# Kernel tuning notes

Measured on AMD Instinct MI355X. Metric: run time of the kernel, lower is better.

The kernel has to match this reference:

```python
import jax, jax.numpy as jnp
import numpy as np

B, N, F, Tf, Tm, Df, Dm = 8, 128, 128, 64, 256, 32, 128
E, H, TE = 64, 128, 64  # node_emb_dim, hidden_dim, time_emb_dim


def setup_inputs() -> dict:
    key = jax.random.key(0)
    ks = jax.random.split(key, 16)
    s = 0.05
    return {
        'noisy_adj': jax.random.normal(ks[0], (B, N, N), jnp.float32),
        'node_feats': jax.random.normal(ks[1], (B, N, F), jnp.float32),
        'feat_fnirs': jax.random.normal(ks[2], (B, N, Tf, Df), jnp.float32),
        'feat_music': jax.random.normal(ks[3], (B, 1, Tm, Dm), jnp.float32),
        'g_pre': jax.random.normal(ks[4], (B, N, N), jnp.float32),
        'node_W': jax.random.normal(ks[5], (F, E), jnp.float32) * s,
        'node_b': jnp.zeros((E,), jnp.float32),
        'fnirs_W': jax.random.normal(ks[6], (Df, H), jnp.float32) * s,
        'fnirs_b': jnp.zeros((H,), jnp.float32),
        'music_W': jax.random.normal(ks[7], (Dm, H), jnp.float32) * s,
        'music_b': jnp.zeros((H,), jnp.float32),
        'mlp_W1': jax.random.normal(ks[8], (2 * E + 2 + H + TE, H), jnp.float32) * s,
        'mlp_b1': jnp.zeros((H,), jnp.float32),
        'mlp_W2': jax.random.normal(ks[9], (H, 1), jnp.float32) * s,
        'mlp_b2': jnp.zeros((1,), jnp.float32),
        't': jax.random.randint(ks[10], (B,), 0, Tf),
    }


def _time_embedding(t_idx):
    # sinusoidal timestep embedding -> [B, TE]
    half = TE // 2
    inv_freq = jnp.exp(-jnp.arange(half, dtype=jnp.float32) * (jnp.log(10000.0) / (half - 1)))
    freqs = t_idx.astype(jnp.float32)[:, None] * inv_freq  # [B, half]
    return jnp.concatenate([jnp.sin(freqs), jnp.cos(freqs)], axis=-1)


def _conditional(feat_fnirs, feat_music, fnirs_W, fnirs_b, music_W, music_b):
    # cross-attention: fNIRS timesteps attend over music timesteps
    q = feat_fnirs @ fnirs_W + fnirs_b          # [B,N,Tf,H]
    kv = feat_music @ music_W + music_b         # [B,1,Tm,H]
    scale = 1.0 / jnp.sqrt(jnp.float32(H))
    scores = jnp.einsum('bnfh,bomh->bnfm', q, kv) * scale  # [B,N,Tf,Tm]
    attn = jax.nn.softmax(scores, axis=-1)
    ctx = jnp.einsum('bnfm,bomh->bnfh', attn, kv)
    fused = q + ctx                              # [B,N,Tf,H]
    attn_weights = attn.mean(axis=1)             # mean across channels -> [B,Tf,Tm]
    ent = -(attn * jnp.log(attn + 1e-8)).sum(-1)
    attention_loss = ent.mean()
    return fused, attn_weights, attention_loss


def reference(noisy_adj, node_feats, feat_fnirs, feat_music, g_pre,
              node_W, node_b, fnirs_W, fnirs_b, music_W, music_b,
              mlp_W1, mlp_b1, mlp_W2, mlp_b2, t):
    h = node_feats @ node_W + node_b             # [B,N,E]

    fused, attn_weights, attention_loss = _conditional(
        feat_fnirs, feat_music, fnirs_W, fnirs_b, music_W, music_b)

    t_idx = jnp.clip(t, 0, fused.shape[2] - 1)
    # gather conditional state at diffusion step t -> [B,N,H]
    idx = jnp.broadcast_to(t_idx[:, None, None, None], (B, N, 1, H))
    cond_t = jnp.take_along_axis(fused, idx, axis=2)[:, :, 0, :]

    time_emb = _time_embedding(t_idx)            # [B,TE]

    # Fused edge MLP layer-1: split W1 along the concat axis instead of
    # materializing the [B,N,N,in_dim] concat tensor (same math).
    W1_hi = mlp_W1[:E]
    W1_hj = mlp_W1[E:2 * E]
    w_adj = mlp_W1[2 * E]          # [H]
    w_gpre = mlp_W1[2 * E + 1]     # [H]
    W1_cond = mlp_W1[2 * E + 2:2 * E + 2 + H]
    W1_time = mlp_W1[2 * E + 2 + H:]

    pre = ((h @ W1_hi)[:, :, None, :]            # h_i varies over row i
           + (h @ W1_hj)[:, None, :, :]          # h_j varies over col j
           + noisy_adj[..., None] * w_adj
           + g_pre[..., None] * w_gpre
           + (cond_t @ W1_cond)[:, None, :, :]   # cond broadcast over row i
           + (time_emb @ W1_time)[:, None, None, :]
           + mlp_b1)                             # [B,N,N,H]
    hid = jax.nn.relu(pre)
    noise_pred = (hid @ mlp_W2)[..., 0] + mlp_b2[0]  # [B,N,N]
    return noise_pred, attn_weights, attention_loss
```

## Files before the change

kernel.cpp:

```cpp
#include <hip/hip_runtime.h>
#include <hip/hip_bf16.h>

#define Bn  8
#define Nn  128
#define Fn  128
#define Tfn 64
#define Tmn 256
#define Dfn 32
#define Dmn 128
#define En  64
#define Hn  128
#define TEn 64

#define OUT_AW_OFF   (Bn*Nn*Nn)
#define OUT_LOSS_OFF (Bn*Nn*Nn + Bn*Tfn*Tmn)

#define WS_KV    0
#define WS_GBF   (WS_KV + Bn*Tmn*Hn)
#define WS_BIAS  (WS_GBF + (Bn*Tmn*Dfn)/2)
#define WS_PI    (WS_BIAS + Bn*Tmn)
#define WS_PJ    (WS_PI + Bn*Nn*Hn)
#define WS_LOSS  (WS_PJ + Bn*Nn*Hn)

#define SCALE 0.08838834764831845f

typedef __attribute__((ext_vector_type(8))) short short8;
typedef __attribute__((ext_vector_type(4))) float f32x4;

__device__ __forceinline__ unsigned short f2bf(float x) {
  __hip_bfloat16 h = __float2bfloat16(x);
  return __builtin_bit_cast(unsigned short, h);
}
__device__ __forceinline__ unsigned int pk2(float a, float b) {
  return (unsigned int)f2bf(a) | ((unsigned int)f2bf(b) << 16);
}
__device__ __forceinline__ float bfl(unsigned int u) {
  union { unsigned int u; float f; } v; v.u = u << 16; return v.f;
}
__device__ __forceinline__ float bfh(unsigned int u) {
  union { unsigned int u; float f; } v; v.u = u & 0xFFFF0000u; return v.f;
}

__global__ __launch_bounds__(128) void k_kv(
    const float* __restrict__ feat_music, const float* __restrict__ music_W,
    const float* __restrict__ music_b, const float* __restrict__ fnirs_W,
    const float* __restrict__ fnirs_b, float* __restrict__ kv,
    unsigned short* __restrict__ G_bf, float* __restrict__ bias,
    float* __restrict__ loss_acc)
{
  int b = blockIdx.x >> 8;
  int m = blockIdx.x & 255;
  int tid = threadIdx.x;
  __shared__ float fm_s[Dmn];
  __shared__ float kv_s[Hn];
  fm_s[tid] = feat_music[((size_t)b*Tmn + m)*Dmn + tid];
  __syncthreads();
  float a = music_b[tid];
  #pragma unroll 8
  for (int d = 0; d < Dmn; d++) a = fmaf(fm_s[d], music_W[d*Hn + tid], a);
  kv[((size_t)b*Tmn + m)*Hn + tid] = a;
  kv_s[tid] = a;
  __syncthreads();
  if (tid < Dfn) {
    float g = 0.f;
    #pragma unroll 8
    for (int h = 0; h < Hn; h++) g = fmaf(fnirs_W[tid*Hn + h], kv_s[h], g);
    G_bf[((size_t)b*Tmn + m)*Dfn + tid] = f2bf(g * SCALE);
  } else if (tid == 64) {
    float g = 0.f;
    #pragma unroll 8
    for (int h = 0; h < Hn; h++) g = fmaf(fnirs_b[h], kv_s[h], g);
    bias[(size_t)b*Tmn + m] = g * SCALE;
  }
  if (blockIdx.x == 0 && tid == 0) loss_acc[0] = 0.f;
}

__global__ __launch_bounds__(256, 2) void k_attn(
    const float* __restrict__ feat_fnirs, const unsigned short* __restrict__ G_bf,
    const float* __restrict__ bias, float* __restrict__ aw_out,
    float* __restrict__ loss_acc)
{
  __shared__ unsigned short feat_l[Nn][40];
  __shared__ unsigned short G_l[Tmn][40];
  __shared__ float bias_l[Tmn];
  __shared__ float aw_l[4][Tmn];
  __shared__ float ent_l[4];

  int tid = threadIdx.x;
  int b = blockIdx.x >> 6, f = blockIdx.x & 63;

  {
    const uint4* gg = (const uint4*)(G_bf + (size_t)b*Tmn*Dfn);
    #pragma unroll
    for (int v0 = 0; v0 < 4; v0++) {
      int v = tid + v0*256;
      uint4 x = gg[v];
      int m = v >> 2, qt = v & 3;
      *((uint4*)&G_l[m][qt*8]) = x;
    }
    bias_l[tid] = bias[b*Tmn + tid];
    int n = tid >> 1, hf = tid & 1;
    const float* src = feat_fnirs + (((size_t)b*Nn + n)*Tfn + f)*Dfn + hf*16;
    float4 x0 = ((const float4*)src)[0];
    float4 x1 = ((const float4*)src)[1];
    float4 x2 = ((const float4*)src)[2];
    float4 x3 = ((const float4*)src)[3];
    uint4 pa, pb;
    pa.x = pk2(x0.x, x0.y); pa.y = pk2(x0.z, x0.w);
    pa.z = pk2(x1.x, x1.y); pa.w = pk2(x1.z, x1.w);
    pb.x = pk2(x2.x, x2.y); pb.y = pk2(x2.z, x2.w);
    pb.z = pk2(x3.x, x3.y); pb.w = pk2(x3.z, x3.w);
    uint4* dst = (uint4*)&feat_l[n][hf*16];
    dst[0] = pa; dst[1] = pb;
  }
  __syncthreads();

  int lane = tid & 63, wv = tid >> 6;
  int col = lane & 15, kq = lane >> 4;
  int n0 = wv * 32;

  short8 a0 = *(const short8*)&feat_l[n0 + col][kq*8];
  short8 a1 = *(const short8*)&feat_l[n0 + 16 + col][kq*8];

  float S0[4] = {0,0,0,0}, S1[4] = {0,0,0,0};
  float T0[4] = {0,0,0,0}, T1[4] = {0,0,0,0};
  float p0[16][4], p1[16][4];

  #pragma unroll
  for (int mt = 0; mt < 16; mt++) {
    short8 bfr = *(const short8*)&G_l[mt*16 + col][kq*8];
    float bv = bias_l[mt*16 + col];
    f32x4 c0 = __builtin_amdgcn_mfma_f32_16x16x32_bf16(a0, bfr, (f32x4){0.f,0.f,0.f,0.f}, 0, 0, 0);
    f32x4 c1 = __builtin_amdgcn_mfma_f32_16x16x32_bf16(a1, bfr, (f32x4){0.f,0.f,0.f,0.f}, 0, 0, 0);
    #pragma unroll
    for (int r = 0; r < 4; r++) {
      float sc = c0[r] + bv;
      float p = __expf(sc);
      S0[r] += p; T0[r] = fmaf(p, sc, T0[r]); p0[mt][r] = p;
      sc = c1[r] + bv;
      p = __expf(sc);
      S1[r] += p; T1[r] = fmaf(p, sc, T1[r]); p1[mt][r] = p;
    }
  }

  #pragma unroll
  for (int r = 0; r < 4; r++) {
    #pragma unroll
    for (int off = 1; off < 16; off <<= 1) {
      S0[r] += __shfl_xor(S0[r], off);
      S1[r] += __shfl_xor(S1[r], off);
      T0[r] += __shfl_xor(T0[r], off);
      T1[r] += __shfl_xor(T1[r], off);
    }
  }
  float i0v[4], i1v[4];
  #pragma unroll
  for (int r = 0; r < 4; r++) { i0v[r] = 1.f / S0[r]; i1v[r] = 1.f / S1[r]; }

  float ent = 0.f;
  if (col == 0) {
    #pragma unroll
    for (int r = 0; r < 4; r++) {
      ent += (__logf(S0[r]) - T0[r] * i0v[r]);
      ent += (__logf(S1[r]) - T1[r] * i1v[r]);
    }
  }
  ent += __shfl_xor(ent, 32); ent += __shfl_xor(ent, 16);
  ent += __shfl_xor(ent, 8);  ent += __shfl_xor(ent, 4);
  ent += __shfl_xor(ent, 2);  ent += __shfl_xor(ent, 1);
  if (lane == 0) ent_l[wv] = ent;

  #pragma unroll
  for (int mt = 0; mt < 16; mt++) {
    float a = 0.f;
    #pragma unroll
    for (int r = 0; r < 4; r++) {
      a = fmaf(p0[mt][r], i0v[r], a);
      a = fmaf(p1[mt][r], i1v[r], a);
    }
    a += __shfl_xor(a, 16);
    a += __shfl_xor(a, 32);
    if (lane < 16) aw_l[wv][mt*16 + lane] = a;
  }
  __syncthreads();

  float s = (aw_l[0][tid] + aw_l[1][tid]) + (aw_l[2][tid] + aw_l[3][tid]);
  aw_out[((size_t)b*Tfn + f)*Tmn + tid] = s * (1.f/(float)Nn);
  if (tid == 0)
    atomicAdd(loss_acc, (ent_l[0] + ent_l[1]) + (ent_l[2] + ent_l[3]));
}

__global__ __launch_bounds__(128) void k_cond(
    const float* __restrict__ feat_fnirs, const float* __restrict__ fnirs_W,
    const float* __restrict__ fnirs_b, const float* __restrict__ kv,
    const unsigned short* __restrict__ G_bf, const float* __restrict__ bias,
    const int* __restrict__ t, const float* __restrict__ node_feats,
    const float* __restrict__ node_W, const float* __restrict__ node_b,
    const float* __restrict__ W1, const float* __restrict__ b1,
    float* __restrict__ Pi, float* __restrict__ Pj)
{
  int b = blockIdx.x >> 7, i = blockIdx.x & 127;
  int tid = threadIdx.x;
  int tcl = min(max(t[b], 0), Tfn - 1);
  __shared__ float feat_s[Dfn], attn_s[Tmn], nf_s[Fn], h_s[En], cond_s[Hn],
                   te_s[TEn], red_s[2];

  nf_s[tid] = node_feats[((size_t)b*Nn + i)*Fn + tid];
  if (tid < Dfn) feat_s[tid] = feat_fnirs[(((size_t)b*Nn + i)*Tfn + tcl)*Dfn + tid];
  if (tid >= 64 && tid < 96) {
    int u = tid - 64;
    float fr = (float)tcl * __expf(-(float)u * (logf(10000.f) / (TEn/2 - 1)));
    te_s[u] = __sinf(fr);
    te_s[u + TEn/2] = __cosf(fr);
  }
  __syncthreads();

  {
    float sc0 = bias[b*Tmn + tid], sc1 = bias[b*Tmn + tid + 128];
    const unsigned short* r0 = G_bf + ((size_t)b*Tmn + tid)*Dfn;
    const unsigned short* r1 = G_bf + ((size_t)b*Tmn + tid + 128)*Dfn;
    #pragma unroll 8
    for (int d = 0; d < Dfn; d += 2) {
      unsigned int w0 = *(const unsigned int*)(r0 + d);
      unsigned int w1 = *(const unsigned int*)(r1 + d);
      sc0 = fmaf(feat_s[d], bfl(w0), sc0); sc0 = fmaf(feat_s[d+1], bfh(w0), sc0);
      sc1 = fmaf(feat_s[d], bfl(w1), sc1); sc1 = fmaf(feat_s[d+1], bfh(w1), sc1);
    }
    float p0 = __expf(sc0), p1 = __expf(sc1);
    float v = p0 + p1;
    v += __shfl_xor(v, 32); v += __shfl_xor(v, 16); v += __shfl_xor(v, 8);
    v += __shfl_xor(v, 4);  v += __shfl_xor(v, 2);  v += __shfl_xor(v, 1);
    if ((tid & 63) == 0) red_s[tid >> 6] = v;
    __syncthreads();
    float invS = 1.f / (red_s[0] + red_s[1]);
    attn_s[tid] = p0 * invS;
    attn_s[tid + 128] = p1 * invS;
  }

  if (tid < En) {
    float a = node_b[tid];
    #pragma unroll 8
    for (int ff = 0; ff < Fn; ff++) a = fmaf(nf_s[ff], node_W[ff*En + tid], a);
    h_s[tid] = a;
  }
  __syncthreads();

  float q = fnirs_b[tid];
  #pragma unroll 8
  for (int d = 0; d < Dfn; d++) q = fmaf(feat_s[d], fnirs_W[d*Hn + tid], q);
  float ctx = 0.f;
  const float* kvb = kv + (size_t)b*Tmn*Hn + tid;
  #pragma unroll 8
  for (int m = 0; m < Tmn; m++) ctx = fmaf(attn_s[m], kvb[(size_t)m*Hn], ctx);
  cond_s[tid] = q + ctx;
  __syncthreads();

  int k = tid;
  float A = 0.f, Bv = 0.f, C = 0.f, Dv = 0.f;
  #pragma unroll 4
  for (int e = 0; e < En; e++) {
    float hv = h_s[e];
    A  = fmaf(hv, W1[e*Hn + k], A);
    Bv = fmaf(hv, W1[(En + e)*Hn + k], Bv);
  }
  #pragma unroll 4
  for (int c = 0; c < Hn; c++) C = fmaf(cond_s[c], W1[(2*En + 2 + c)*Hn + k], C);
  #pragma unroll 4
  for (int u = 0; u < TEn; u++) Dv = fmaf(te_s[u], W1[(2*En + 2 + Hn + u)*Hn + k], Dv);
  Pi[((size_t)b*Nn + i)*Hn + k] = A;
  Pj[((size_t)b*Nn + i)*Hn + k] = Bv + C + Dv + b1[k];
}

__global__ __launch_bounds__(256) void k_edge(
    const float* __restrict__ adj, const float* __restrict__ gpre,
    const float* __restrict__ W1, const float* __restrict__ W2,
    const float* __restrict__ b2p, const float* __restrict__ Pi,
    const float* __restrict__ Pj, float* __restrict__ out,
    const float* __restrict__ loss_acc)
{
  int b  = blockIdx.x >> 6;
  int ib = (blockIdx.x >> 1) & 31;
  int jh = blockIdx.x & 1;
  int i0 = ib * 4;
  int tid = threadIdx.x;

  __shared__ float4 Pj_s4[64*32];
  __shared__ float4 Pi_s4[4*32];
  __shared__ float4 w2_s[32], wa_s[32], wg_s[32];

  {
    const float4* Pjg = (const float4*)(Pj + ((size_t)b*Nn + jh*64)*Hn);
    #pragma unroll
    for (int v0 = 0; v0 < 8; v0++) {
      int idx = tid + v0*256;
      int j = idx >> 5, c = idx & 31;
      Pj_s4[j*32 + (c ^ (j & 7))] = Pjg[j*32 + c];
    }
    if (tid < 128) {
      int r = tid >> 5, c = tid & 31;
      Pi_s4[r*32 + c] = ((const float4*)(Pi + ((size_t)b*Nn + i0 + r)*Hn))[c];
    } else if (tid < 160) {
      int c = tid - 128;
      w2_s[c] = ((const float4*)W2)[c];
      wa_s[c] = ((const float4*)(W1 + (2*En)*Hn))[c];
      wg_s[c] = ((const float4*)(W1 + (2*En + 1)*Hn))[c];
    }
  }
  __syncthreads();

  int r = tid >> 6, lane = tid & 63;
  int i = i0 + r, j = jh*64 + lane;
  float b2v = b2p[0];
  float adjv = adj [((size_t)b*Nn + i)*Nn + j];
  float gpv  = gpre[((size_t)b*Nn + i)*Nn + j];
  float a0 = 0.f, a1 = 0.f, a2 = 0.f, a3 = 0.f;
  #pragma unroll
  for (int c = 0; c < 32; c++) {
    float4 pj = Pj_s4[lane*32 + (c ^ (lane & 7))];
    float4 pi = Pi_s4[r*32 + c];
    float4 wa = wa_s[c], wg = wg_s[c], w2 = w2_s[c];
    float e0 = pi.x + pj.x + adjv*wa.x + gpv*wg.x;
    float e1 = pi.y + pj.y + adjv*wa.y + gpv*wg.y;
    float e2 = pi.z + pj.z + adjv*wa.z + gpv*wg.z;
    float e3 = pi.w + pj.w + adjv*wa.w + gpv*wg.w;
    a0 = fmaf(fmaxf(e0, 0.f), w2.x, a0);
    a1 = fmaf(fmaxf(e1, 0.f), w2.y, a1);
    a2 = fmaf(fmaxf(e2, 0.f), w2.z, a2);
    a3 = fmaf(fmaxf(e3, 0.f), w2.w, a3);
  }
  out[((size_t)b*Nn + i)*Nn + j] = (a0 + a1) + (a2 + a3) + b2v;

  if (blockIdx.x == 0 && tid == 0)
    out[OUT_LOSS_OFF] = loss_acc[0] * (1.f / (float)(Bn*Nn*Tfn));
}

extern "C" void kernel_launch(void* const* d_in, const int* in_sizes, int n_in,
                              void* d_out, int out_size, void* d_ws, size_t ws_size,
                              hipStream_t stream) {
  (void)in_sizes; (void)n_in; (void)out_size; (void)ws_size;
  const float* noisy_adj  = (const float*)d_in[0];
  const float* node_feats = (const float*)d_in[1];
  const float* feat_fnirs = (const float*)d_in[2];
  const float* feat_music = (const float*)d_in[3];
  const float* g_pre      = (const float*)d_in[4];
  const float* node_W     = (const float*)d_in[5];
  const float* node_b     = (const float*)d_in[6];
  const float* fnirs_W    = (const float*)d_in[7];
  const float* fnirs_b    = (const float*)d_in[8];
  const float* music_W    = (const float*)d_in[9];
  const float* music_b    = (const float*)d_in[10];
  const float* mlp_W1     = (const float*)d_in[11];
  const float* mlp_b1     = (const float*)d_in[12];
  const float* mlp_W2     = (const float*)d_in[13];
  const float* mlp_b2     = (const float*)d_in[14];
  const int*   t          = (const int*)d_in[15];

  float* out = (float*)d_out;
  float* ws = (float*)d_ws;
  float*          kv_ws   = ws + WS_KV;
  unsigned short* gbf_ws  = (unsigned short*)(ws + WS_GBF);
  float*          bias_ws = ws + WS_BIAS;
  float*          Pi_ws   = ws + WS_PI;
  float*          Pj_ws   = ws + WS_PJ;
  float*          loss_ws = ws + WS_LOSS;

  k_kv  <<<Bn*Tmn, 128, 0, stream>>>(feat_music, music_W, music_b, fnirs_W,
                                     fnirs_b, kv_ws, gbf_ws, bias_ws, loss_ws);
  k_attn<<<Bn*Tfn, 256, 0, stream>>>(feat_fnirs, gbf_ws, bias_ws,
                                     out + OUT_AW_OFF, loss_ws);
  k_cond<<<Bn*Nn,  128, 0, stream>>>(feat_fnirs, fnirs_W, fnirs_b, kv_ws,
                                     gbf_ws, bias_ws, t, node_feats, node_W,
                                     node_b, mlp_W1, mlp_b1, Pi_ws, Pj_ws);
  k_edge<<<512,    256, 0, stream>>>(noisy_adj, g_pre, mlp_W1, mlp_W2, mlp_b2,
                                     Pi_ws, Pj_ws, out, loss_ws);
}
```

Measured before the change: 158.6 us.

## Rewrite conditional projection kernel with bf16 MFMA over 16-node tiles

Replaces the per-node scalar k_cond with a 16-node tile kernel that uses bf16 MFMA for the scores, the softmax-weighted context, the node embedding and the W1 projections. A new prep kernel transposes and casts the weights to bf16 and precomputes the time-embedding term. k_kv now writes a transposed bf16 kv and parallelises the G/bias reductions across more threads. The aim is to cut the scalar FMA work and the repeated weight reads in k_cond, at the cost of an extra launch and bf16 rounding of cond and h.

```diff
diff --git a/kernel.cpp b/kernel.cpp
--- a/kernel.cpp
+++ b/kernel.cpp
@@ -15,12 +15,18 @@
 #define OUT_AW_OFF   (Bn*Nn*Nn)
 #define OUT_LOSS_OFF (Bn*Nn*Nn + Bn*Tfn*Tmn)
 
-#define WS_KV    0
-#define WS_GBF   (WS_KV + Bn*Tmn*Hn)
-#define WS_BIAS  (WS_GBF + (Bn*Tmn*Dfn)/2)
-#define WS_PI    (WS_BIAS + Bn*Tmn)
-#define WS_PJ    (WS_PI + Bn*Nn*Hn)
-#define WS_LOSS  (WS_PJ + Bn*Nn*Hn)
+#define WS_G     0
+#define WS_BIAS  32768
+#define WS_KVT   34816
+#define WS_FWT   165888
+#define WS_NWT   167936
+#define WS_HIT   172032
+#define WS_HJT   176128
+#define WS_CONDT 180224
+#define WS_TVEC  188416
+#define WS_PI    189440
+#define WS_PJ    320512
+#define WS_LOSS  451584
 
 #define SCALE 0.08838834764831845f
 
@@ -34,45 +40,108 @@
 __device__ __forceinline__ unsigned int pk2(float a, float b) {
   return (unsigned int)f2bf(a) | ((unsigned int)f2bf(b) << 16);
 }
-__device__ __forceinline__ float bfl(unsigned int u) {
-  union { unsigned int u; float f; } v; v.u = u << 16; return v.f;
-}
-__device__ __forceinline__ float bfh(unsigned int u) {
-  union { unsigned int u; float f; } v; v.u = u & 0xFFFF0000u; return v.f;
+
+__global__ __launch_bounds__(128) void k_wprep(
+    const float* __restrict__ W1, const float* __restrict__ b1,
+    const float* __restrict__ node_W, const float* __restrict__ fnirs_W,
+    const int* __restrict__ t,
+    unsigned short* __restrict__ fwt, unsigned short* __restrict__ nwt,
+    unsigned short* __restrict__ hit, unsigned short* __restrict__ hjt,
+    unsigned short* __restrict__ condt, float* __restrict__ tvec,
+    float* __restrict__ loss_acc)
+{
+  int blk = blockIdx.x, tid = threadIdx.x;
+  if (blk < 8) {
+    int b = blk;
+    __shared__ float te_l[TEn];
+    if (tid < TEn/2) {
+      int tcl = min(max(t[b], 0), Tfn - 1);
+      float fr = (float)tcl * __expf(-(float)tid * (logf(10000.f) / (TEn/2 - 1)));
+      te_l[tid] = __sinf(fr);
+      te_l[tid + TEn/2] = __cosf(fr);
+    }
+    __syncthreads();
+    float a = b1[tid];
+    #pragma unroll 8
+    for (int u = 0; u < TEn; u++) a = fmaf(te_l[u], W1[(2*En + 2 + Hn + u)*Hn + tid], a);
+    tvec[b*Hn + tid] = a;
+    if (b == 0 && tid == 0) loss_acc[0] = 0.f;
+  } else if (blk < 16) {
+    int q = blk - 8;
+    #pragma unroll 4
+    for (int i = 0; i < 16; i++) {
+      int k = q*16 + i;
+      condt[k*Hn + tid] = f2bf(W1[(2*En + 2 + tid)*Hn + k]);
+    }
+  } else if (blk < 20) {
+    int q = blk - 16;
+    int e = tid & 63, kh = tid >> 6;
+    #pragma unroll 4
+    for (int i = 0; i < 16; i++) {
+      int k = q*32 + kh*16 + i;
+      hit[k*En + e] = f2bf(W1[e*Hn + k]);
+    }
+  } else if (blk < 24) {
+    int q = blk - 20;
+    int e = tid & 63, kh = tid >> 6;
+    #pragma unroll 4
+    for (int i = 0; i < 16; i++) {
+      int k = q*32 + kh*16 + i;
+      hjt[k*En + e] = f2bf(W1[(En + e)*Hn + k]);
+    }
+  } else if (blk < 32) {
+    int q = blk - 24;
+    int fl = tid & 15, eh = tid >> 4;
+    #pragma unroll 4
+    for (int i = 0; i < 8; i++) {
+      int e = eh*8 + i;
+      nwt[e*Fn + q*16 + fl] = f2bf(node_W[(q*16 + fl)*En + e]);
+    }
+  } else if (blk < 34) {
+    int q = blk - 32;
+    int d = tid & 31, hh = tid >> 5;
+    #pragma unroll 4
+    for (int i = 0; i < 16; i++) {
+      int h = q*64 + hh*16 + i;
+      fwt[h*Dfn + d] = f2bf(fnirs_W[d*Hn + h]);
+    }
+  }
 }
 
 __global__ __launch_bounds__(128) void k_kv(
     const float* __restrict__ feat_music, const float* __restrict__ music_W,
     const float* __restrict__ music_b, const float* __restrict__ fnirs_W,
-    const float* __restrict__ fnirs_b, float* __restrict__ kv,
-    unsigned short* __restrict__ G_bf, float* __restrict__ bias,
-    float* __restrict__ loss_acc)
+    const float* __restrict__ fnirs_b, unsigned short* __restrict__ kvT,
+    unsigned short* __restrict__ G_bf, float* __restrict__ bias)
 {
   int b = blockIdx.x >> 8;
   int m = blockIdx.x & 255;
   int tid = threadIdx.x;
   __shared__ float fm_s[Dmn];
   __shared__ float kv_s[Hn];
+  __shared__ float red[2];
   fm_s[tid] = feat_music[((size_t)b*Tmn + m)*Dmn + tid];
   __syncthreads();
   float a = music_b[tid];
   #pragma unroll 8
   for (int d = 0; d < Dmn; d++) a = fmaf(fm_s[d], music_W[d*Hn + tid], a);
-  kv[((size_t)b*Tmn + m)*Hn + tid] = a;
   kv_s[tid] = a;
-  __syncthreads();
-  if (tid < Dfn) {
-    float g = 0.f;
-    #pragma unroll 8
-    for (int h = 0; h < Hn; h++) g = fmaf(fnirs_W[tid*Hn + h], kv_s[h], g);
-    G_bf[((size_t)b*Tmn + m)*Dfn + tid] = f2bf(g * SCALE);
-  } else if (tid == 64) {
-    float g = 0.f;
-    #pragma unroll 8
-    for (int h = 0; h < Hn; h++) g = fmaf(fnirs_b[h], kv_s[h], g);
-    bias[(size_t)b*Tmn + m] = g * SCALE;
-  }
-  if (blockIdx.x == 0 && tid == 0) loss_acc[0] = 0.f;
+  kvT[((size_t)b*Hn + tid)*Tmn + m] = f2bf(a);
+  float bp = fnirs_b[tid] * a;
+  bp += __shfl_xor(bp, 32); bp += __shfl_xor(bp, 16); bp += __shfl_xor(bp, 8);
+  bp += __shfl_xor(bp, 4);  bp += __shfl_xor(bp, 2);  bp += __shfl_xor(bp, 1);
+  if ((tid & 63) == 0) red[tid >> 6] = bp;
+  __syncthreads();
+  int d = tid >> 2, qd = tid & 3;
+  float g = 0.f;
+  #pragma unroll 8
+  for (int hh = 0; hh < 32; hh++) {
+    int h = hh*4 + qd;
+    g = fmaf(fnirs_W[d*Hn + h], kv_s[h], g);
+  }
+  g += __shfl_xor(g, 1); g += __shfl_xor(g, 2);
+  if (qd == 0) G_bf[((size_t)b*Tmn + m)*Dfn + d] = f2bf(g * SCALE);
+  if (tid == 0) bias[b*Tmn + m] = (red[0] + red[1]) * SCALE;
 }
 
 __global__ __launch_bounds__(256, 2) void k_attn(
@@ -190,85 +259,152 @@
     atomicAdd(loss_acc, (ent_l[0] + ent_l[1]) + (ent_l[2] + ent_l[3]));
 }
 
-__global__ __launch_bounds__(128) void k_cond(
-    const float* __restrict__ feat_fnirs, const float* __restrict__ fnirs_W,
-    const float* __restrict__ fnirs_b, const float* __restrict__ kv,
+__global__ __launch_bounds__(256) void k_cond(
+    const float* __restrict__ feat_fnirs, const float* __restrict__ node_feats,
+    const float* __restrict__ node_b, const int* __restrict__ t,
     const unsigned short* __restrict__ G_bf, const float* __restrict__ bias,
-    const int* __restrict__ t, const float* __restrict__ node_feats,
-    const float* __restrict__ node_W, const float* __restrict__ node_b,
-    const float* __restrict__ W1, const float* __restrict__ b1,
-    float* __restrict__ Pi, float* __restrict__ Pj)
+    const unsigned short* __restrict__ kvT, const unsigned short* __restrict__ fwt,
+    const unsigned short* __restrict__ nwt, const unsigned short* __restrict__ hit,
+    const unsigned short* __restrict__ hjt, const unsigned short* __restrict__ condt,
+    const float* __restrict__ tvec, float* __restrict__ Pi, float* __restrict__ Pj)
 {
-  int b = blockIdx.x >> 7, i = blockIdx.x & 127;
+  __shared__ unsigned short featT_l[16][40];
+  __shared__ unsigned short A_l[16][264];
+  __shared__ unsigned short nf_l[16][136];
+  __shared__ unsigned short h_l[16][72];
+  __shared__ unsigned short cond_l[16][136];
+  __shared__ float sS[4][16];
+  __shared__ float tvec_l[Hn];
+
   int tid = threadIdx.x;
+  int b = blockIdx.x >> 3;
+  int i0 = (blockIdx.x & 7) << 4;
   int tcl = min(max(t[b], 0), Tfn - 1);
-  __shared__ float feat_s[Dfn], attn_s[Tmn], nf_s[Fn], h_s[En], cond_s[Hn],
-                   te_s[TEn], red_s[2];
-
-  nf_s[tid] = node_feats[((size_t)b*Nn + i)*Fn + tid];
-  if (tid < Dfn) feat_s[tid] = feat_fnirs[(((size_t)b*Nn + i)*Tfn + tcl)*Dfn + tid];
-  if (tid >= 64 && tid < 96) {
-    int u = tid - 64;
-    float fr = (float)tcl * __expf(-(float)u * (logf(10000.f) / (TEn/2 - 1)));
-    te_s[u] = __sinf(fr);
-    te_s[u + TEn/2] = __cosf(fr);
-  }
-  __syncthreads();
-
+
+  if (tid < 128) {
+    int i = tid >> 3, c = (tid & 7) * 4;
+    const float* src = feat_fnirs + (((size_t)b*Nn + i0 + i)*Tfn + tcl)*Dfn + c;
+    float4 x = *(const float4*)src;
+    *(unsigned int*)&featT_l[i][c]     = pk2(x.x, x.y);
+    *(unsigned int*)&featT_l[i][c + 2] = pk2(x.z, x.w);
+    tvec_l[tid] = tvec[b*Hn + tid];
+  }
   {
-    float sc0 = bias[b*Tmn + tid], sc1 = bias[b*Tmn + tid + 128];
-    const unsigned short* r0 = G_bf + ((size_t)b*Tmn + tid)*Dfn;
-    const unsigned short* r1 = G_bf + ((size_t)b*Tmn + tid + 128)*Dfn;
-    #pragma unroll 8
-    for (int d = 0; d < Dfn; d += 2) {
-      unsigned int w0 = *(const unsigned int*)(r0 + d);
-      unsigned int w1 = *(const unsigned int*)(r1 + d);
-      sc0 = fmaf(feat_s[d], bfl(w0), sc0); sc0 = fmaf(feat_s[d+1], bfh(w0), sc0);
-      sc1 = fmaf(feat_s[d], bfl(w1), sc1); sc1 = fmaf(feat_s[d+1], bfh(w1), sc1);
-    }
-    float p0 = __expf(sc0), p1 = __expf(sc1);
-    float v = p0 + p1;
-    v += __shfl_xor(v, 32); v += __shfl_xor(v, 16); v += __shfl_xor(v, 8);
-    v += __shfl_xor(v, 4);  v += __shfl_xor(v, 2);  v += __shfl_xor(v, 1);
-    if ((tid & 63) == 0) red_s[tid >> 6] = v;
-    __syncthreads();
-    float invS = 1.f / (red_s[0] + red_s[1]);
-    attn_s[tid] = p0 * invS;
-    attn_s[tid + 128] = p1 * invS;
-  }
-
-  if (tid < En) {
-    float a = node_b[tid];
-    #pragma unroll 8
-    for (int ff = 0; ff < Fn; ff++) a = fmaf(nf_s[ff], node_W[ff*En + tid], a);
-    h_s[tid] = a;
-  }
-  __syncthreads();
-
-  float q = fnirs_b[tid];
-  #pragma unroll 8
-  for (int d = 0; d < Dfn; d++) q = fmaf(feat_s[d], fnirs_W[d*Hn + tid], q);
-  float ctx = 0.f;
-  const float* kvb = kv + (size_t)b*Tmn*Hn + tid;
-  #pragma unroll 8
-  for (int m = 0; m < Tmn; m++) ctx = fmaf(attn_s[m], kvb[(size_t)m*Hn], ctx);
-  cond_s[tid] = q + ctx;
-  __syncthreads();
-
-  int k = tid;
-  float A = 0.f, Bv = 0.f, C = 0.f, Dv = 0.f;
-  #pragma unroll 4
-  for (int e = 0; e < En; e++) {
-    float hv = h_s[e];
-    A  = fmaf(hv, W1[e*Hn + k], A);
-    Bv = fmaf(hv, W1[(En + e)*Hn + k], Bv);
-  }
-  #pragma unroll 4
-  for (int c = 0; c < Hn; c++) C = fmaf(cond_s[c], W1[(2*En + 2 + c)*Hn + k], C);
-  #pragma unroll 4
-  for (int u = 0; u < TEn; u++) Dv = fmaf(te_s[u], W1[(2*En + 2 + Hn + u)*Hn + k], Dv);
-  Pi[((size_t)b*Nn + i)*Hn + k] = A;
-  Pj[((size_t)b*Nn + i)*Hn + k] = Bv + C + Dv + b1[k];
+    int i = tid >> 4, c = (tid & 15) * 8;
+    const float* src = node_feats + ((size_t)b*Nn + i0 + i)*Fn + c;
+    float4 x0 = ((const float4*)src)[0];
+    float4 x1 = ((const float4*)src)[1];
+    *(unsigned int*)&nf_l[i][c]     = pk2(x0.x, x0.y);
+    *(unsigned int*)&nf_l[i][c + 2] = pk2(x0.z, x0.w);
+    *(unsigned int*)&nf_l[i][c + 4] = pk2(x1.x, x1.y);
+    *(unsigned int*)&nf_l[i][c + 6] = pk2(x1.z, x1.w);
+  }
+  __syncthreads();
+
+  int lane = tid & 63, wv = tid >> 6;
+  int col = lane & 15, kq = lane >> 4;
+
+  short8 a_feat = *(const short8*)&featT_l[col][kq*8];
+
+  float p[4][4];
+  float Sp[4] = {0,0,0,0};
+  #pragma unroll
+  for (int mtl = 0; mtl < 4; mtl++) {
+    int mt = wv*4 + mtl;
+    short8 bg = *(const short8*)(G_bf + ((size_t)b*Tmn + mt*16 + col)*Dfn + kq*8);
+    f32x4 c = __builtin_amdgcn_mfma_f32_16x16x32_bf16(a_feat, bg, (f32x4){0.f,0.f,0.f,0.f}, 0, 0, 0);
+    float bv = bias[b*Tmn + mt*16 + col];
+    #pragma unroll
+    for (int r = 0; r < 4; r++) {
+      float pp = __expf(c[r] + bv);
+      p[mtl][r] = pp;
+      Sp[r] += pp;
+    }
+  }
+  #pragma unroll
+  for (int r = 0; r < 4; r++) {
+    float v = Sp[r];
+    v += __shfl_xor(v, 1); v += __shfl_xor(v, 2);
+    v += __shfl_xor(v, 4); v += __shfl_xor(v, 8);
+    Sp[r] = v;
+  }
+  if (col == 0) {
+    #pragma unroll
+    for (int r = 0; r < 4; r++) sS[wv][kq*4 + r] = Sp[r];
+  }
+  __syncthreads();
+  float invS[4];
+  #pragma unroll
+  for (int r = 0; r < 4; r++)
+    invS[r] = 1.f / (sS[0][kq*4+r] + sS[1][kq*4+r] + sS[2][kq*4+r] + sS[3][kq*4+r]);
+  #pragma unroll
+  for (int mtl = 0; mtl < 4; mtl++) {
+    #pragma unroll
+    for (int r = 0; r < 4; r++)
+      A_l[kq*4 + r][(wv*4 + mtl)*16 + col] = f2bf(p[mtl][r] * invS[r]);
+  }
+  __syncthreads();
+
+  f32x4 accC0 = {0.f,0.f,0.f,0.f}, accC1 = {0.f,0.f,0.f,0.f};
+  {
+    int ct0 = wv*2, ct1 = wv*2 + 1;
+    short8 bq0 = *(const short8*)(fwt + (size_t)(ct0*16 + col)*Dfn + kq*8);
+    short8 bq1 = *(const short8*)(fwt + (size_t)(ct1*16 + col)*Dfn + kq*8);
+    accC0 = __builtin_amdgcn_mfma_f32_16x16x32_bf16(a_feat, bq0, accC0, 0, 0, 0);
+    accC1 = __builtin_amdgcn_mfma_f32_16x16x32_bf16(a_feat, bq1, accC1, 0, 0, 0);
+    #pragma unroll
+    for (int ks = 0; ks < 8; ks++) {
+      short8 aA = *(const short8*)&A_l[col][ks*32 + kq*8];
+      short8 bk0 = *(const short8*)(kvT + ((size_t)b*Hn + ct0*16 + col)*Tmn + ks*32 + kq*8);
+      short8 bk1 = *(const short8*)(kvT + ((size_t)b*Hn + ct1*16 + col)*Tmn + ks*32 + kq*8);
+      accC0 = __builtin_amdgcn_mfma_f32_16x16x32_bf16(aA, bk0, accC0, 0, 0, 0);
+      accC1 = __builtin_amdgcn_mfma_f32_16x16x32_bf16(aA, bk1, accC1, 0, 0, 0);
+    }
+  }
+  f32x4 accH = {0.f,0.f,0.f,0.f};
+  #pragma unroll
+  for (int ks = 0; ks < 4; ks++) {
+    short8 aN = *(const short8*)&nf_l[col][ks*32 + kq*8];
+    short8 bn = *(const short8*)(nwt + (size_t)(wv*16 + col)*Fn + ks*32 + kq*8);
+    accH = __builtin_amdgcn_mfma_f32_16x16x32_bf16(aN, bn, accH, 0, 0, 0);
+  }
+  float nb = node_b[wv*16 + col];
+  #pragma unroll
+  for (int r = 0; r < 4; r++) {
+    cond_l[kq*4 + r][(wv*2    )*16 + col] = f2bf(accC0[r]);
+    cond_l[kq*4 + r][(wv*2 + 1)*16 + col] = f2bf(accC1[r]);
+    h_l[kq*4 + r][wv*16 + col] = f2bf(accH[r] + nb);
+  }
+  __syncthreads();
+
+  short8 aH[2];
+  aH[0] = *(const short8*)&h_l[col][kq*8];
+  aH[1] = *(const short8*)&h_l[col][32 + kq*8];
+  #pragma unroll
+  for (int ctl = 0; ctl < 2; ctl++) {
+    int ct = wv*2 + ctl;
+    f32x4 accPi = {0.f,0.f,0.f,0.f}, accPj = {0.f,0.f,0.f,0.f};
+    #pragma unroll
+    for (int ks = 0; ks < 2; ks++) {
+      short8 bi_ = *(const short8*)(hit + (size_t)(ct*16 + col)*En + ks*32 + kq*8);
+      short8 bj_ = *(const short8*)(hjt + (size_t)(ct*16 + col)*En + ks*32 + kq*8);
+      accPi = __builtin_amdgcn_mfma_f32_16x16x32_bf16(aH[ks], bi_, accPi, 0, 0, 0);
+      accPj = __builtin_amdgcn_mfma_f32_16x16x32_bf16(aH[ks], bj_, accPj, 0, 0, 0);
+    }
+    #pragma unroll
+    for (int ks = 0; ks < 4; ks++) {
+      short8 aC = *(const short8*)&cond_l[col][ks*32 + kq*8];
+      short8 bc = *(const short8*)(condt + (size_t)(ct*16 + col)*Hn + ks*32 + kq*8);
+      accPj = __builtin_amdgcn_mfma_f32_16x16x32_bf16(aC, bc, accPj, 0, 0, 0);
+    }
+    float tv = tvec_l[ct*16 + col];
+    #pragma unroll
+    for (int r = 0; r < 4; r++) {
+      size_t row = (size_t)b*Nn + i0 + kq*4 + r;
+      Pi[row*Hn + ct*16 + col] = accPi[r];
+      Pj[row*Hn + ct*16 + col] = accPj[r] + tv;
+    }
+  }
 }
 
 __global__ __launch_bounds__(256) void k_edge(
@@ -357,20 +493,30 @@
 
   float* out = (float*)d_out;
   float* ws = (float*)d_ws;
-  float*          kv_ws   = ws + WS_KV;
-  unsigned short* gbf_ws  = (unsigned short*)(ws + WS_GBF);
+  unsigned short* g_ws    = (unsigned short*)(ws + WS_G);
   float*          bias_ws = ws + WS_BIAS;
+  unsigned short* kvt_ws  = (unsigned short*)(ws + WS_KVT);
+  unsigned short* fwt_ws  = (unsigned short*)(ws + WS_FWT);
+  unsigned short* nwt_ws  = (unsigned short*)(ws + WS_NWT);
+  unsigned short* hit_ws  = (unsigned short*)(ws + WS_HIT);
+  unsigned short* hjt_ws  = (unsigned short*)(ws + WS_HJT);
+  unsigned short* cndt_ws = (unsigned short*)(ws + WS_CONDT);
+  float*          tvec_ws = ws + WS_TVEC;
   float*          Pi_ws   = ws + WS_PI;
   float*          Pj_ws   = ws + WS_PJ;
   float*          loss_ws = ws + WS_LOSS;
 
-  k_kv  <<<Bn*Tmn, 128, 0, stream>>>(feat_music, music_W, music_b, fnirs_W,
-                                     fnirs_b, kv_ws, gbf_ws, bias_ws, loss_ws);
-  k_attn<<<Bn*Tfn, 256, 0, stream>>>(feat_fnirs, gbf_ws, bias_ws,
-                                     out + OUT_AW_OFF, loss_ws);
-  k_cond<<<Bn*Nn,  128, 0, stream>>>(feat_fnirs, fnirs_W, fnirs_b, kv_ws,
-                                     gbf_ws, bias_ws, t, node_feats, node_W,
-                                     node_b, mlp_W1, mlp_b1, Pi_ws, Pj_ws);
-  k_edge<<<512,    256, 0, stream>>>(noisy_adj, g_pre, mlp_W1, mlp_W2, mlp_b2,
-                                     Pi_ws, Pj_ws, out, loss_ws);
-}
+  k_wprep<<<34,         128, 0, stream>>>(mlp_W1, mlp_b1, node_W, fnirs_W, t,
+                                          fwt_ws, nwt_ws, hit_ws, hjt_ws, cndt_ws,
+                                          tvec_ws, loss_ws);
+  k_kv   <<<Bn*Tmn,     128, 0, stream>>>(feat_music, music_W, music_b, fnirs_W,
+                                          fnirs_b, kvt_ws, g_ws, bias_ws);
+  k_attn <<<Bn*Tfn,     256, 0, stream>>>(feat_fnirs, g_ws, bias_ws,
+                                          out + OUT_AW_OFF, loss_ws);
+  k_cond <<<Bn*(Nn/16), 256, 0, stream>>>(feat_fnirs, node_feats, node_b, t,
+                                          g_ws, bias_ws, kvt_ws, fwt_ws, nwt_ws,
+                                          hit_ws, hjt_ws, cndt_ws, tvec_ws,
+                                          Pi_ws, Pj_ws);
+  k_edge <<<512,        256, 0, stream>>>(noisy_adj, g_pre, mlp_W1, mlp_W2, mlp_b2,
+                                          Pi_ws, Pj_ws, out, loss_ws);
+}
```

New measurement: 137.1 us. 13.6% less time.
